# Kernel tuning notes

Hardware: AMD Instinct MI355X
Metric: run time of the kernel (lower is better)

Reference implementation:

```python
import jax, jax.numpy as jnp
import numpy as np

HIDDEN = 2048
N_HEADS = 16
N_KV_HEADS = 8
HEAD_DIM = 128  # == head_dim_original, no padding needed
ROPE_THETA = 1000000.0
EPS = 1e-6
T_NOISE = 512
T_CTX = 1536
MAX_KV = 8192


def rms_norm(x, scale, eps=EPS):
    # normalize over last axis (head_dim), per-head like nnx.RMSNorm(head_dim)
    var = jnp.mean(x * x, axis=-1, keepdims=True)
    return x * jax.lax.rsqrt(var + eps) * scale


def apply_rope(x, positions, head_dim=HEAD_DIM, theta=ROPE_THETA):
    # x: (T, N, H), positions: (T,) int
    inv_freq = 1.0 / (theta ** (jnp.arange(0, head_dim, 2, dtype=jnp.float32) / head_dim))
    ang = positions.astype(jnp.float32)[:, None] * inv_freq  # (T, H/2)
    cos = jnp.cos(ang)[:, None, :]  # (T, 1, H/2)
    sin = jnp.sin(ang)[:, None, :]
    x1, x2 = jnp.split(x, 2, axis=-1)
    return jnp.concatenate([x1 * cos - x2 * sin, x2 * cos + x1 * sin], axis=-1).astype(x.dtype)


def setup_inputs() -> dict:
    key = jax.random.key(0)
    ks = jax.random.split(key, 10)
    s = 0.02
    return {
        "x_noise": jax.random.normal(ks[0], (T_NOISE, HIDDEN), jnp.float32),
        "target_hidden": jax.random.normal(ks[1], (T_CTX, HIDDEN), jnp.float32),
        "noise_positions": jnp.arange(T_NOISE, dtype=jnp.int32) + T_CTX,
        "ctx_positions": jnp.arange(T_CTX, dtype=jnp.int32),
        "kv_cache_k": jax.random.normal(ks[2], (1, N_HEADS, MAX_KV, HEAD_DIM), jnp.float32),
        "kv_cache_v": jax.random.normal(ks[3], (1, N_HEADS, MAX_KV, HEAD_DIM), jnp.float32),
        "cache_len": 2048,
        "wq": jax.random.normal(ks[4], (HIDDEN, N_HEADS, HEAD_DIM), jnp.float32) * s,
        "wk": jax.random.normal(ks[5], (HIDDEN, N_KV_HEADS, HEAD_DIM), jnp.float32) * s,
        "wv": jax.random.normal(ks[6], (HIDDEN, N_KV_HEADS, HEAD_DIM), jnp.float32) * s,
        "wo": jax.random.normal(ks[7], (N_HEADS, HEAD_DIM, HIDDEN), jnp.float32) * s,
        "q_scale": jnp.ones((HEAD_DIM,), jnp.float32) + jax.random.uniform(ks[8], (HEAD_DIM,), jnp.float32, -0.05, 0.05),
        "k_scale": jnp.ones((HEAD_DIM,), jnp.float32) + jax.random.uniform(ks[9], (HEAD_DIM,), jnp.float32, -0.05, 0.05),
    }


def reference(x_noise, target_hidden, noise_positions, ctx_positions, kv_cache_k,
              kv_cache_v, cache_len, wq, wk, wv, wo, q_scale, k_scale):
    num_kv_groups = N_HEADS // N_KV_HEADS
    t_noise = x_noise.shape[0]

    # 1. Q projection + RMSNorm + RoPE
    q = jnp.einsum('td,dnh->tnh', x_noise, wq)
    q = rms_norm(q, q_scale)
    q = apply_rope(q, noise_positions)

    # 2. K/V over [context, noise]
    x_new = jnp.concatenate([target_hidden, x_noise], axis=0)  # (T_new, D)
    k_new = jnp.einsum('td,dkh->tkh', x_new, wk)
    v_new = jnp.einsum('td,dkh->tkh', x_new, wv)
    k_new = rms_norm(k_new, k_scale)
    new_positions = jnp.concatenate([ctx_positions, noise_positions], axis=0)
    k_new = apply_rope(k_new, new_positions)

    # 3. GQA head repeat
    if num_kv_groups > 1:
        k_new = jnp.repeat(k_new, num_kv_groups, axis=1)
        v_new = jnp.repeat(v_new, num_kv_groups, axis=1)

    # 4. Scatter new K/V into cache at dynamic offset cache_len
    t_new = x_new.shape[0]
    k_new_4d = k_new.transpose(1, 0, 2)[None]  # (1, N, T_new, H)
    v_new_4d = v_new.transpose(1, 0, 2)[None]
    kv_cache_k = jax.lax.dynamic_update_slice(kv_cache_k, k_new_4d, (0, 0, cache_len, 0))
    kv_cache_v = jax.lax.dynamic_update_slice(kv_cache_v, v_new_4d, (0, 0, cache_len, 0))
    new_cache_len = cache_len + t_new
    max_kv = kv_cache_k.shape[2]

    # 5. Non-causal attention over valid cache (segment-id mask = valid length)
    q_4d = q.transpose(1, 0, 2)[None]  # (1, N, T_noise, H)
    sm_scale = HEAD_DIM ** -0.5
    scores = jnp.einsum('bnth,bnsh->bnts', q_4d, kv_cache_k) * sm_scale  # (1,N,Tq,S)
    valid = jnp.arange(max_kv) < new_cache_len  # (S,)
    scores = jnp.where(valid[None, None, None, :], scores, jnp.float32(-1e30))
    probs = jax.nn.softmax(scores, axis=-1)
    attn = jnp.einsum('bnts,bnsh->bnth', probs, kv_cache_v)
    attn = attn[0].transpose(1, 0, 2)  # (T_noise, N, H)

    output = jnp.einsum('tnh,nhd->td', attn, wo)
    return output, kv_cache_k, kv_cache_v
```

## Files before the change

kernel.cpp:

```cpp
#include <hip/hip_runtime.h>
#include <hip/hip_bf16.h>

#define HIDDEN 2048
#define NH 16
#define NKV 8
#define HD 128
#define TN 512
#define TC 1536
#define TNEW 2048
#define MAXKV 8192

using u16 = unsigned short;
using u32 = unsigned int;

typedef short short8 __attribute__((ext_vector_type(8)));
typedef float floatx4 __attribute__((ext_vector_type(4)));

__device__ __forceinline__ u16 f2bf(float f) {
  u32 u = __float_as_uint(f);
  u += 0x7FFFu + ((u >> 16) & 1u);
  return (u16)(u >> 16);
}

__device__ __forceinline__ uint4 pack8(const float* f) {
  uint4 r;
  r.x = (u32)f2bf(f[0]) | ((u32)f2bf(f[1]) << 16);
  r.y = (u32)f2bf(f[2]) | ((u32)f2bf(f[3]) << 16);
  r.z = (u32)f2bf(f[4]) | ((u32)f2bf(f[5]) << 16);
  r.w = (u32)f2bf(f[6]) | ((u32)f2bf(f[7]) << 16);
  return r;
}

__device__ __forceinline__ short8 ldfrag(const u16* p) {
  uint4 v = *(const uint4*)p;
  return __builtin_bit_cast(short8, v);
}

__global__ __launch_bounds__(256) void cache_copy(
    const float4* __restrict__ inK, const float4* __restrict__ inV,
    float4* __restrict__ outK, float4* __restrict__ outV,
    const int* __restrict__ clp)
{
  const int cl = *clp;
  long long idx = (long long)blockIdx.x * 256 + threadIdx.x;
  const long long per = (long long)NH * MAXKV * (HD / 4);
  const float4* src = inK;
  float4* dst = outK;
  long long r = idx;
  if (r >= per) { r -= per; src = inV; dst = outV; }
  int row = (int)((r >> 5) & (MAXKV - 1));
  if (row >= cl && row < cl + TNEW) return;
  dst[r] = src[r];
}

__global__ __launch_bounds__(256) void gemm_bf16(
    const float* __restrict__ A0, int rows0, const float* __restrict__ A1,
    const float* __restrict__ B0, const float* __restrict__ B1, int Nhalf,
    float* __restrict__ C0, float* __restrict__ C1,
    int M, int N, int K, int ksteps)
{
  __shared__ u16 As[64 * 40];
  __shared__ u16 Bs[64 * 40];
  const int tid = threadIdx.x;
  const int lane = tid & 63;
  const int wave = tid >> 6;
  const int quad = lane >> 4;
  const int m16 = lane & 15;
  const int bm = blockIdx.y * 64;
  const int bn = blockIdx.x * 64;
  const int wm = (wave >> 1) * 32;
  const int wn = (wave & 1) * 32;
  const int z = blockIdx.z;
  const int kbase = z * ksteps * 32;

  const float* B = (bn < Nhalf) ? B0 : B1;
  float*       C = (bn < Nhalf) ? C0 : C1;
  const int n0 = (bn < Nhalf) ? bn : bn - Nhalf;
  const int strideN = (bn < Nhalf) ? Nhalf : (N - Nhalf);

  floatx4 acc[2][2];
#pragma unroll
  for (int i = 0; i < 2; i++)
#pragma unroll
    for (int j = 0; j < 2; j++)
#pragma unroll
      for (int r = 0; r < 4; r++) acc[i][j][r] = 0.0f;

  const int arow = tid >> 2, akg = (tid & 3) * 8;
  const int brow = tid >> 3, bng = (tid & 7) * 8;
  const int garow = bm + arow;
  const float* Ap = (garow < rows0) ? (A0 + (size_t)garow * K)
                                    : (A1 + (size_t)(garow - rows0) * K);

  for (int ks = 0; ks < ksteps; ks++) {
    const int k0 = kbase + ks * 32;
    if (k0 >= K) break;
    float av[8];
    *(float4*)(av)     = *(const float4*)(Ap + k0 + akg);
    *(float4*)(av + 4) = *(const float4*)(Ap + k0 + akg + 4);
    *(uint4*)&As[arow * 40 + akg] = pack8(av);

    float bv[8];
    const float* Bp = B + (size_t)(k0 + brow) * strideN + n0 + bng;
    *(float4*)(bv)     = *(const float4*)(Bp);
    *(float4*)(bv + 4) = *(const float4*)(Bp + 4);
#pragma unroll
    for (int j = 0; j < 8; j++) Bs[(bng + j) * 40 + brow] = f2bf(bv[j]);

    __syncthreads();

    short8 a0 = ldfrag(&As[(wm + m16) * 40 + quad * 8]);
    short8 a1 = ldfrag(&As[(wm + 16 + m16) * 40 + quad * 8]);
    short8 b0 = ldfrag(&Bs[(wn + m16) * 40 + quad * 8]);
    short8 b1 = ldfrag(&Bs[(wn + 16 + m16) * 40 + quad * 8]);
    acc[0][0] = __builtin_amdgcn_mfma_f32_16x16x32_bf16(a0, b0, acc[0][0], 0, 0, 0);
    acc[0][1] = __builtin_amdgcn_mfma_f32_16x16x32_bf16(a0, b1, acc[0][1], 0, 0, 0);
    acc[1][0] = __builtin_amdgcn_mfma_f32_16x16x32_bf16(a1, b0, acc[1][0], 0, 0, 0);
    acc[1][1] = __builtin_amdgcn_mfma_f32_16x16x32_bf16(a1, b1, acc[1][1], 0, 0, 0);

    __syncthreads();
  }

  const size_t zoff = (size_t)z * M * Nhalf;
#pragma unroll
  for (int mt = 0; mt < 2; mt++)
#pragma unroll
    for (int nt = 0; nt < 2; nt++)
#pragma unroll
      for (int r = 0; r < 4; r++) {
        int row = bm + wm + mt * 16 + quad * 4 + r;
        int col = wn + nt * 16 + m16;
        C[zoff + (size_t)row * strideN + n0 + col] = acc[mt][nt][r];
      }
}

__global__ __launch_bounds__(256) void reduce4(
    const float4* __restrict__ P, float4* __restrict__ C, int n4)
{
  int idx = blockIdx.x * 256 + threadIdx.x;
  if (idx >= n4) return;
  float4 a = P[idx], b = P[idx + n4], c = P[idx + 2 * n4], d = P[idx + 3 * n4];
  float4 r;
  r.x = (a.x + b.x) + (c.x + d.x);
  r.y = (a.y + b.y) + (c.y + d.y);
  r.z = (a.z + b.z) + (c.z + d.z);
  r.w = (a.w + b.w) + (c.w + d.w);
  C[idx] = r;
}

__global__ __launch_bounds__(64) void q_post_k(
    const float* __restrict__ qproj, const int* __restrict__ npos,
    const float* __restrict__ qscale, u16* __restrict__ qbf)
{
  const int t = blockIdx.x, n = blockIdx.y, i = threadIdx.x;
  const size_t base = (size_t)t * HIDDEN + n * HD;
  const float x1 = qproj[base + i];
  const float x2 = qproj[base + i + 64];
  float ss = x1 * x1 + x2 * x2;
#pragma unroll
  for (int m = 1; m < 64; m <<= 1) ss += __shfl_xor(ss, m, 64);
  const float rstd = rsqrtf(ss * (1.0f / HD) + 1e-6f);
  float y1 = x1 * rstd * qscale[i];
  float y2 = x2 * rstd * qscale[i + 64];
  const float pos = (float)npos[t];
  const float ang = pos * exp2f(-(float)i * (19.931568569324174f / 64.0f));
  const float c = cosf(ang), s = sinf(ang);
  const float sc = 0.08838834764831845f * 1.4426950408889634f;
  qbf[base + i]      = f2bf((y1 * c - y2 * s) * sc);
  qbf[base + i + 64] = f2bf((y2 * c + y1 * s) * sc);
}

__global__ __launch_bounds__(64) void k_post_k(
    const float* __restrict__ kproj, const int* __restrict__ ctxpos,
    const int* __restrict__ npos, const float* __restrict__ kscale,
    const int* __restrict__ clp, float* __restrict__ outK)
{
  const int t = blockIdx.x, kh = blockIdx.y, i = threadIdx.x;
  const int cl = *clp;
  const size_t base = (size_t)t * (NKV * HD) + kh * HD;
  const float x1 = kproj[base + i];
  const float x2 = kproj[base + i + 64];
  float ss = x1 * x1 + x2 * x2;
#pragma unroll
  for (int m = 1; m < 64; m <<= 1) ss += __shfl_xor(ss, m, 64);
  const float rstd = rsqrtf(ss * (1.0f / HD) + 1e-6f);
  float y1 = x1 * rstd * kscale[i];
  float y2 = x2 * rstd * kscale[i + 64];
  const int posi = (t < TC) ? ctxpos[t] : npos[t - TC];
  const float ang = (float)posi * exp2f(-(float)i * (19.931568569324174f / 64.0f));
  const float c = cosf(ang), s = sinf(ang);
  const float o1 = y1 * c - y2 * s;
  const float o2 = y2 * c + y1 * s;
  const size_t row = (size_t)cl + t;
  const size_t b0 = ((size_t)(2 * kh) * MAXKV + row) * HD;
  const size_t b1 = ((size_t)(2 * kh + 1) * MAXKV + row) * HD;
  outK[b0 + i] = o1; outK[b0 + i + 64] = o2;
  outK[b1 + i] = o1; outK[b1 + i + 64] = o2;
}

__global__ __launch_bounds__(128) void v_post_k(
    const float* __restrict__ vproj, const int* __restrict__ clp,
    float* __restrict__ outV)
{
  const int t = blockIdx.x, kh = blockIdx.y, h = threadIdx.x;
  const int cl = *clp;
  const float v = vproj[(size_t)t * (NKV * HD) + kh * HD + h];
  const size_t row = (size_t)cl + t;
  outV[((size_t)(2 * kh) * MAXKV + row) * HD + h] = v;
  outV[((size_t)(2 * kh + 1) * MAXKV + row) * HD + h] = v;
}

__global__ __launch_bounds__(256) void attn_k(
    const u16* __restrict__ qbf, const float* __restrict__ outK,
    const float* __restrict__ outV, const int* __restrict__ clp,
    float* __restrict__ Opart, float* __restrict__ Oml)
{
  __shared__ u16 Ks[32 * 136];
  __shared__ u16 Vt[128 * 40];
  __shared__ u16 Ps[4 * 16 * 40];
  const int tid = threadIdx.x;
  const int lane = tid & 63, wave = tid >> 6;
  const int quad = lane >> 4, m16 = lane & 15;
  const int head = blockIdx.y;
  const int qbase = blockIdx.x * 64 + wave * 16;
  const int z = blockIdx.z, splits = gridDim.z;
  const int Svalid = *clp + TNEW;
  const int ntiles = (Svalid + 31) >> 5;
  const int per = (ntiles + splits - 1) / splits;
  const int it0 = z * per;
  const int it1 = min(ntiles, it0 + per);

  short8 qf[4];
#pragma unroll
  for (int kb = 0; kb < 4; kb++)
    qf[kb] = ldfrag(&qbf[((size_t)(qbase + m16) * NH + head) * HD + kb * 32 + quad * 8]);

  floatx4 O[8];
#pragma unroll
  for (int i = 0; i < 8; i++)
#pragma unroll
    for (int r = 0; r < 4; r++) O[i][r] = 0.0f;
  float mrow[4], lrow[4];
#pragma unroll
  for (int r = 0; r < 4; r++) { mrow[r] = -1e30f; lrow[r] = 0.0f; }

  const int sstage = tid >> 3;
  const int hg = (tid & 7) * 16;

  for (int it = it0; it < it1; it++) {
    const int s0 = it * 32;
    {
      int srow = s0 + sstage; if (srow > MAXKV - 1) srow = MAXKV - 1;
      const float* kp = outK + ((size_t)head * MAXKV + srow) * HD + hg;
      float tv[16];
      *(float4*)(tv)      = *(const float4*)(kp);
      *(float4*)(tv + 4)  = *(const float4*)(kp + 4);
      *(float4*)(tv + 8)  = *(const float4*)(kp + 8);
      *(float4*)(tv + 12) = *(const float4*)(kp + 12);
      *(uint4*)&Ks[sstage * 136 + hg]     = pack8(tv);
      *(uint4*)&Ks[sstage * 136 + hg + 8] = pack8(tv + 8);
      const float* vp = outV + ((size_t)head * MAXKV + srow) * HD + hg;
      float vv[16];
      *(float4*)(vv)      = *(const float4*)(vp);
      *(float4*)(vv + 4)  = *(const float4*)(vp + 4);
      *(float4*)(vv + 8)  = *(const float4*)(vp + 8);
      *(float4*)(vv + 12) = *(const float4*)(vp + 12);
#pragma unroll
      for (int j = 0; j < 16; j++) Vt[(hg + j) * 40 + sstage] = f2bf(vv[j]);
    }
    __syncthreads();

    floatx4 sc[2];
#pragma unroll
    for (int st = 0; st < 2; st++) {
      floatx4 a;
#pragma unroll
      for (int r = 0; r < 4; r++) a[r] = 0.0f;
#pragma unroll
      for (int kb = 0; kb < 4; kb++) {
        short8 kf = ldfrag(&Ks[(st * 16 + m16) * 136 + kb * 32 + quad * 8]);
        a = __builtin_amdgcn_mfma_f32_16x16x32_bf16(qf[kb], kf, a, 0, 0, 0);
      }
      const int scol = s0 + st * 16 + m16;
      if (scol >= Svalid) {
#pragma unroll
        for (int r = 0; r < 4; r++) a[r] = -1e30f;
      }
      sc[st] = a;
    }

    float alpha[4];
#pragma unroll
    for (int r = 0; r < 4; r++) {
      float mx = fmaxf(sc[0][r], sc[1][r]);
      mx = fmaxf(mx, __shfl_xor(mx, 1, 64));
      mx = fmaxf(mx, __shfl_xor(mx, 2, 64));
      mx = fmaxf(mx, __shfl_xor(mx, 4, 64));
      mx = fmaxf(mx, __shfl_xor(mx, 8, 64));
      const float mn = fmaxf(mrow[r], mx);
      alpha[r] = exp2f(mrow[r] - mn);
      const float p0 = exp2f(sc[0][r] - mn);
      const float p1 = exp2f(sc[1][r] - mn);
      sc[0][r] = p0; sc[1][r] = p1;
      float rs = p0 + p1;
      rs += __shfl_xor(rs, 1, 64);
      rs += __shfl_xor(rs, 2, 64);
      rs += __shfl_xor(rs, 4, 64);
      rs += __shfl_xor(rs, 8, 64);
      lrow[r] = lrow[r] * alpha[r] + rs;
      mrow[r] = mn;
    }
#pragma unroll
    for (int hb = 0; hb < 8; hb++)
#pragma unroll
      for (int r = 0; r < 4; r++) O[hb][r] *= alpha[r];

    u16* myPs = &Ps[wave * 640];
#pragma unroll
    for (int st = 0; st < 2; st++)
#pragma unroll
      for (int r = 0; r < 4; r++)
        myPs[(quad * 4 + r) * 40 + st * 16 + m16] = f2bf(sc[st][r]);
    short8 pf = ldfrag(&myPs[m16 * 40 + quad * 8]);
#pragma unroll
    for (int hb = 0; hb < 8; hb++) {
      short8 vf = ldfrag(&Vt[(hb * 16 + m16) * 40 + quad * 8]);
      O[hb] = __builtin_amdgcn_mfma_f32_16x16x32_bf16(pf, vf, O[hb], 0, 0, 0);
    }
    __syncthreads();
  }

  const size_t zbase = (size_t)z * TN * NH;
  const int trow = qbase + quad * 4;
#pragma unroll
  for (int hb = 0; hb < 8; hb++)
#pragma unroll
    for (int r = 0; r < 4; r++)
      Opart[(zbase + (size_t)(trow + r) * NH + head) * HD + hb * 16 + m16] = O[hb][r];
  if (m16 == 0) {
#pragma unroll
    for (int r = 0; r < 4; r++) {
      Oml[(zbase + (size_t)(trow + r) * NH + head) * 2 + 0] = mrow[r];
      Oml[(zbase + (size_t)(trow + r) * NH + head) * 2 + 1] = lrow[r];
    }
  }
}

__global__ __launch_bounds__(128) void attn_combine(
    const float* __restrict__ Opart, const float* __restrict__ Oml,
    float* __restrict__ attnb, int splits)
{
  const int pair = blockIdx.x;
  const int h = threadIdx.x;
  float M = -1e30f;
  for (int zz = 0; zz < splits; zz++)
    M = fmaxf(M, Oml[((size_t)zz * TN * NH + pair) * 2]);
  float l = 0.0f, o = 0.0f;
  for (int zz = 0; zz < splits; zz++) {
    const float mi = Oml[((size_t)zz * TN * NH + pair) * 2];
    const float li = Oml[((size_t)zz * TN * NH + pair) * 2 + 1];
    const float w = exp2f(mi - M);
    l += li * w;
    o += Opart[((size_t)zz * TN * NH + pair) * HD + h] * w;
  }
  attnb[(size_t)pair * HD + h] = o / l;
}

extern "C" void kernel_launch(void* const* d_in, const int* in_sizes, int n_in,
                              void* d_out, int out_size, void* d_ws, size_t ws_size,
                              hipStream_t stream) {
  const float* x_noise       = (const float*)d_in[0];
  const float* target_hidden = (const float*)d_in[1];
  const int*   noise_pos     = (const int*)d_in[2];
  const int*   ctx_pos       = (const int*)d_in[3];
  const float* inK           = (const float*)d_in[4];
  const float* inV           = (const float*)d_in[5];
  const int*   cache_len     = (const int*)d_in[6];
  const float* wq            = (const float*)d_in[7];
  const float* wk            = (const float*)d_in[8];
  const float* wv            = (const float*)d_in[9];
  const float* wo            = (const float*)d_in[10];
  const float* q_scale       = (const float*)d_in[11];
  const float* k_scale       = (const float*)d_in[12];

  float* out0 = (float*)d_out;
  float* outK = out0 + (size_t)TN * HIDDEN;
  float* outV = outK + (size_t)NH * MAXKV * HD;

  size_t off = 0;
  auto walloc = [&](size_t bytes) -> void* {
    void* p = (char*)d_ws + off;
    off += (bytes + 255) & ~(size_t)255;
    return p;
  };
  u16*   qbf   = (u16*)walloc((size_t)TN * HIDDEN * 2);
  float* attnb = (float*)walloc((size_t)TN * HIDDEN * 4);
  float* qproj = (float*)walloc((size_t)TN * HIDDEN * 4);
  float* kproj = (float*)walloc((size_t)TNEW * NKV * HD * 4);
  float* vproj = (float*)walloc((size_t)TNEW * NKV * HD * 4);
  float* scratch = (float*)((char*)d_ws + off);
  const size_t avail = (ws_size > off) ? (ws_size - off) : 0;

  const size_t per_split = (size_t)TN * NH * HD * 4 + (size_t)TN * NH * 8;
  int asplits = 2;
  if (avail >= 8 * per_split) asplits = 8;
  else if (avail >= 4 * per_split) asplits = 4;
  float* Opart = scratch;
  float* Oml   = Opart + (size_t)asplits * TN * NH * HD;

  const bool ksplit = (avail >= (size_t)4 * TN * HIDDEN * 4);
  float* gpart = scratch;

  cache_copy<<<dim3(32768), dim3(256), 0, stream>>>(
      (const float4*)inK, (const float4*)inV, (float4*)outK, (float4*)outV, cache_len);

  if (ksplit) {
    gemm_bf16<<<dim3(HIDDEN / 64, TN / 64, 4), dim3(256), 0, stream>>>(
        x_noise, TN, x_noise, wq, wq, HIDDEN, gpart, gpart, TN, HIDDEN, HIDDEN, 16);
    reduce4<<<dim3((TN * HIDDEN / 4 + 255) / 256), dim3(256), 0, stream>>>(
        (const float4*)gpart, (float4*)qproj, TN * HIDDEN / 4);
  } else {
    gemm_bf16<<<dim3(HIDDEN / 64, TN / 64, 1), dim3(256), 0, stream>>>(
        x_noise, TN, x_noise, wq, wq, HIDDEN, qproj, qproj, TN, HIDDEN, HIDDEN, 64);
  }

  gemm_bf16<<<dim3(2 * NKV * HD / 64, TNEW / 64, 1), dim3(256), 0, stream>>>(
      target_hidden, TC, x_noise, wk, wv, NKV * HD, kproj, vproj,
      TNEW, 2 * NKV * HD, HIDDEN, 64);

  q_post_k<<<dim3(TN, NH), dim3(64), 0, stream>>>(qproj, noise_pos, q_scale, qbf);
  k_post_k<<<dim3(TNEW, NKV), dim3(64), 0, stream>>>(
      kproj, ctx_pos, noise_pos, k_scale, cache_len, outK);
  v_post_k<<<dim3(TNEW, NKV), dim3(128), 0, stream>>>(vproj, cache_len, outV);

  attn_k<<<dim3(TN / 64, NH, asplits), dim3(256), 0, stream>>>(
      qbf, outK, outV, cache_len, Opart, Oml);
  attn_combine<<<dim3(TN * NH), dim3(128), 0, stream>>>(Opart, Oml, attnb, asplits);

  if (ksplit) {
    gemm_bf16<<<dim3(HIDDEN / 64, TN / 64, 4), dim3(256), 0, stream>>>(
        attnb, TN, attnb, wo, wo, HIDDEN, gpart, gpart, TN, HIDDEN, HIDDEN, 16);
    reduce4<<<dim3((TN * HIDDEN / 4 + 255) / 256), dim3(256), 0, stream>>>(
        (const float4*)gpart, (float4*)out0, TN * HIDDEN / 4);
  } else {
    gemm_bf16<<<dim3(HIDDEN / 64, TN / 64, 1), dim3(256), 0, stream>>>(
        attnb, TN, attnb, wo, wo, HIDDEN, out0, out0, TN, HIDDEN, HIDDEN, 64);
  }
}
```

Baseline: 556.4 us.

## Build bf16 K and transposed-V shadow caches and use double-buffered async attention

The cache copy and the K/V post-processing kernels now also write bf16 shadow copies of the cache: K stays row-major and V is transposed. A new attention kernel streams these shadows straight into LDS with global_load_lds, double-buffered with manual waitcnt and barriers, an XOR-swizzled K layout and a remapped block order for locality. This halves attention read traffic and removes the per-tile fp32-to-bf16 conversion and transpose. The cost is extra shadow writes, scattered 2-byte transposed V stores in the copy kernel, and a workspace requirement large enough for two shadow buffers, with a fallback to the old path when it is not available.

```diff
diff --git a/kernel.cpp b/kernel.cpp
--- a/kernel.cpp
+++ b/kernel.cpp
@@ -36,21 +36,46 @@
   return __builtin_bit_cast(short8, v);
 }
 
+__device__ __forceinline__ void gload16(const void* g, void* l) {
+  __builtin_amdgcn_global_load_lds(
+      (const __attribute__((address_space(1))) u32*)g,
+      (__attribute__((address_space(3))) u32*)l, 16, 0, 0);
+}
+
 __global__ __launch_bounds__(256) void cache_copy(
     const float4* __restrict__ inK, const float4* __restrict__ inV,
     float4* __restrict__ outK, float4* __restrict__ outV,
-    const int* __restrict__ clp)
+    const int* __restrict__ clp, u16* __restrict__ Kb, u16* __restrict__ VbT)
 {
   const int cl = *clp;
   long long idx = (long long)blockIdx.x * 256 + threadIdx.x;
   const long long per = (long long)NH * MAXKV * (HD / 4);
-  const float4* src = inK;
-  float4* dst = outK;
+  const float4* src; float4* dst; bool isv;
   long long r = idx;
-  if (r >= per) { r -= per; src = inV; dst = outV; }
+  if (r < per) { src = inK; dst = outK; isv = false; }
+  else { r -= per; src = inV; dst = outV; isv = true; }
   int row = (int)((r >> 5) & (MAXKV - 1));
   if (row >= cl && row < cl + TNEW) return;
-  dst[r] = src[r];
+  float4 v = src[r];
+  dst[r] = v;
+  if (row < cl) {
+    if (!isv) {
+      if (Kb) {
+        uint2 p;
+        p.x = (u32)f2bf(v.x) | ((u32)f2bf(v.y) << 16);
+        p.y = (u32)f2bf(v.z) | ((u32)f2bf(v.w) << 16);
+        *(uint2*)(Kb + (size_t)r * 4) = p;
+      }
+    } else if (VbT) {
+      int head = (int)(r >> 18);
+      int h0 = ((int)r & 31) * 4;
+      size_t basev = ((size_t)head * HD + h0) * MAXKV + row;
+      VbT[basev]             = f2bf(v.x);
+      VbT[basev + MAXKV]     = f2bf(v.y);
+      VbT[basev + 2 * MAXKV] = f2bf(v.z);
+      VbT[basev + 3 * MAXKV] = f2bf(v.w);
+    }
+  }
 }
 
 __global__ __launch_bounds__(256) void gemm_bf16(
@@ -173,7 +198,7 @@
 __global__ __launch_bounds__(64) void k_post_k(
     const float* __restrict__ kproj, const int* __restrict__ ctxpos,
     const int* __restrict__ npos, const float* __restrict__ kscale,
-    const int* __restrict__ clp, float* __restrict__ outK)
+    const int* __restrict__ clp, float* __restrict__ outK, u16* __restrict__ Kb)
 {
   const int t = blockIdx.x, kh = blockIdx.y, i = threadIdx.x;
   const int cl = *clp;
@@ -196,11 +221,16 @@
   const size_t b1 = ((size_t)(2 * kh + 1) * MAXKV + row) * HD;
   outK[b0 + i] = o1; outK[b0 + i + 64] = o2;
   outK[b1 + i] = o1; outK[b1 + i + 64] = o2;
+  if (Kb) {
+    const u16 s1 = f2bf(o1), s2 = f2bf(o2);
+    Kb[b0 + i] = s1; Kb[b0 + i + 64] = s2;
+    Kb[b1 + i] = s1; Kb[b1 + i + 64] = s2;
+  }
 }
 
 __global__ __launch_bounds__(128) void v_post_k(
     const float* __restrict__ vproj, const int* __restrict__ clp,
-    float* __restrict__ outV)
+    float* __restrict__ outV, u16* __restrict__ VbT)
 {
   const int t = blockIdx.x, kh = blockIdx.y, h = threadIdx.x;
   const int cl = *clp;
@@ -208,6 +238,174 @@
   const size_t row = (size_t)cl + t;
   outV[((size_t)(2 * kh) * MAXKV + row) * HD + h] = v;
   outV[((size_t)(2 * kh + 1) * MAXKV + row) * HD + h] = v;
+  if (VbT) {
+    const u16 vb = f2bf(v);
+    VbT[((size_t)(2 * kh) * HD + h) * MAXKV + row] = vb;
+    VbT[((size_t)(2 * kh + 1) * HD + h) * MAXKV + row] = vb;
+  }
+}
+
+__global__ __launch_bounds__(256) void attn_sh(
+    const u16* __restrict__ qbf, const u16* __restrict__ Kb,
+    const u16* __restrict__ VbT, const int* __restrict__ clp,
+    float* __restrict__ Opart, float* __restrict__ Oml, int splits)
+{
+  __shared__ u16 Ks[2][32 * 128];
+  __shared__ u16 Vt[2][128 * 32];
+  __shared__ u16 Ps[4][16 * 40];
+
+  const int tid = threadIdx.x;
+  const int lane = tid & 63, wave = tid >> 6;
+  const int quad = lane >> 4, m16 = lane & 15;
+
+  const int lin = blockIdx.x;
+  const int ppx = (NH * splits) >> 3;
+  const int c = lin & 7;
+  const int jj = lin >> 3;
+  const int pair = c * ppx + (jj % ppx);
+  const int x = jj / ppx;
+  const int head = pair & (NH - 1);
+  const int z = pair >> 4;
+
+  const int qbase = x * 64 + wave * 16;
+  const int Svalid = *clp + TNEW;
+  const int ntiles = (Svalid + 31) >> 5;
+  const int per = (ntiles + splits - 1) / splits;
+  const int it0 = z * per;
+  const int it1 = (ntiles < it0 + per) ? ntiles : (it0 + per);
+
+  short8 qf[4];
+#pragma unroll
+  for (int kb = 0; kb < 4; kb++)
+    qf[kb] = ldfrag(&qbf[((size_t)(qbase + m16) * NH + head) * HD + kb * 32 + quad * 8]);
+
+  floatx4 O[8];
+#pragma unroll
+  for (int i = 0; i < 8; i++)
+#pragma unroll
+    for (int r = 0; r < 4; r++) O[i][r] = 0.0f;
+  float mrow[4], lrow[4];
+#pragma unroll
+  for (int r = 0; r < 4; r++) { mrow[r] = -1e30f; lrow[r] = 0.0f; }
+
+  const int krow = tid >> 4;
+  const int ksrccol = ((tid & 15) * 16) ^ ((krow & 7) << 4);
+  const char* Kbase = (const char*)(Kb + (size_t)head * MAXKV * HD);
+  const int vh = tid >> 2;
+  const int vs8 = (tid & 3) * 8;
+  const char* Vbase = (const char*)(VbT + (size_t)head * HD * MAXKV);
+  u16* myPs = &Ps[wave][0];
+  const int kxor = (m16 & 7) << 4;
+  const int wb = wave * 512;
+
+  int b = 0;
+  if (it0 < it1) {
+    {
+      const int s0 = it0 * 32;
+      gload16(Kbase + ((size_t)(s0 + krow) << 8) + ksrccol,          &Ks[0][wb]);
+      gload16(Kbase + ((size_t)(s0 + krow + 16) << 8) + ksrccol,     &Ks[0][2048 + wb]);
+      gload16(Vbase + (((size_t)vh * MAXKV + s0 + vs8) << 1),        &Vt[0][wb]);
+      gload16(Vbase + (((size_t)(vh + 64) * MAXKV + s0 + vs8) << 1), &Vt[0][2048 + wb]);
+    }
+    for (int it = it0; it < it1; ++it) {
+      if (it + 1 < it1) {
+        const int s1 = (it + 1) * 32;
+        u16* KsN = &Ks[b ^ 1][0];
+        u16* VtN = &Vt[b ^ 1][0];
+        gload16(Kbase + ((size_t)(s1 + krow) << 8) + ksrccol,          KsN + wb);
+        gload16(Kbase + ((size_t)(s1 + krow + 16) << 8) + ksrccol,     KsN + 2048 + wb);
+        gload16(Vbase + (((size_t)vh * MAXKV + s1 + vs8) << 1),        VtN + wb);
+        gload16(Vbase + (((size_t)(vh + 64) * MAXKV + s1 + vs8) << 1), VtN + 2048 + wb);
+        asm volatile("s_waitcnt vmcnt(4) lgkmcnt(0)" ::: "memory");
+      } else {
+        asm volatile("s_waitcnt vmcnt(0) lgkmcnt(0)" ::: "memory");
+      }
+      __builtin_amdgcn_s_barrier();
+      __builtin_amdgcn_sched_barrier(0);
+
+      const u16* KsB = &Ks[b][0];
+      const u16* VtB = &Vt[b][0];
+      const int s0 = it * 32;
+
+      floatx4 sc[2];
+#pragma unroll
+      for (int st = 0; st < 2; st++) {
+        floatx4 a;
+#pragma unroll
+        for (int r = 0; r < 4; r++) a[r] = 0.0f;
+        const int rofs = (st * 16 + m16) * 128;
+#pragma unroll
+        for (int kb = 0; kb < 4; kb++) {
+          short8 kf = ldfrag(&KsB[rofs + (((kb * 64 + quad * 16) ^ kxor) >> 1)]);
+          a = __builtin_amdgcn_mfma_f32_16x16x32_bf16(qf[kb], kf, a, 0, 0, 0);
+        }
+        const int scol = s0 + st * 16 + m16;
+        if (scol >= Svalid) {
+#pragma unroll
+          for (int r = 0; r < 4; r++) a[r] = -1e30f;
+        }
+        sc[st] = a;
+      }
+
+      float alpha[4];
+#pragma unroll
+      for (int r = 0; r < 4; r++) {
+        float mx = fmaxf(sc[0][r], sc[1][r]);
+        mx = fmaxf(mx, __shfl_xor(mx, 1, 64));
+        mx = fmaxf(mx, __shfl_xor(mx, 2, 64));
+        mx = fmaxf(mx, __shfl_xor(mx, 4, 64));
+        mx = fmaxf(mx, __shfl_xor(mx, 8, 64));
+        const float mn = fmaxf(mrow[r], mx);
+        alpha[r] = exp2f(mrow[r] - mn);
+        const float p0 = exp2f(sc[0][r] - mn);
+        const float p1 = exp2f(sc[1][r] - mn);
+        sc[0][r] = p0; sc[1][r] = p1;
+        float rs = p0 + p1;
+        rs += __shfl_xor(rs, 1, 64);
+        rs += __shfl_xor(rs, 2, 64);
+        rs += __shfl_xor(rs, 4, 64);
+        rs += __shfl_xor(rs, 8, 64);
+        lrow[r] = lrow[r] * alpha[r] + rs;
+        mrow[r] = mn;
+      }
+#pragma unroll
+      for (int hb = 0; hb < 8; hb++)
+#pragma unroll
+        for (int r = 0; r < 4; r++) O[hb][r] *= alpha[r];
+
+#pragma unroll
+      for (int st = 0; st < 2; st++)
+#pragma unroll
+        for (int r = 0; r < 4; r++)
+          myPs[(quad * 4 + r) * 40 + st * 16 + m16] = f2bf(sc[st][r]);
+      short8 pfr = ldfrag(&myPs[m16 * 40 + quad * 8]);
+#pragma unroll
+      for (int hb = 0; hb < 8; hb++) {
+        short8 vf = ldfrag(&VtB[(hb * 16 + m16) * 32 + quad * 8]);
+        O[hb] = __builtin_amdgcn_mfma_f32_16x16x32_bf16(pfr, vf, O[hb], 0, 0, 0);
+      }
+
+      asm volatile("s_waitcnt lgkmcnt(0)" ::: "memory");
+      __builtin_amdgcn_s_barrier();
+      __builtin_amdgcn_sched_barrier(0);
+      b ^= 1;
+    }
+  }
+
+  const size_t zbase = (size_t)z * TN * NH;
+  const int trow = qbase + quad * 4;
+#pragma unroll
+  for (int hb = 0; hb < 8; hb++)
+#pragma unroll
+    for (int r = 0; r < 4; r++)
+      Opart[(zbase + (size_t)(trow + r) * NH + head) * HD + hb * 16 + m16] = O[hb][r];
+  if (m16 == 0) {
+#pragma unroll
+    for (int r = 0; r < 4; r++) {
+      Oml[(zbase + (size_t)(trow + r) * NH + head) * 2 + 0] = mrow[r];
+      Oml[(zbase + (size_t)(trow + r) * NH + head) * 2 + 1] = lrow[r];
+    }
+  }
 }
 
 __global__ __launch_bounds__(256) void attn_k(
@@ -215,9 +413,9 @@
     const float* __restrict__ outV, const int* __restrict__ clp,
     float* __restrict__ Opart, float* __restrict__ Oml)
 {
-  __shared__ u16 Ks[32 * 136];
-  __shared__ u16 Vt[128 * 40];
-  __shared__ u16 Ps[4 * 16 * 40];
+  __shared__ u16 Ksl[32 * 136];
+  __shared__ u16 Vtl[128 * 40];
+  __shared__ u16 Psl[4 * 16 * 40];
   const int tid = threadIdx.x;
   const int lane = tid & 63, wave = tid >> 6;
   const int quad = lane >> 4, m16 = lane & 15;
@@ -257,8 +455,8 @@
       *(float4*)(tv + 4)  = *(const float4*)(kp + 4);
       *(float4*)(tv + 8)  = *(const float4*)(kp + 8);
       *(float4*)(tv + 12) = *(const float4*)(kp + 12);
-      *(uint4*)&Ks[sstage * 136 + hg]     = pack8(tv);
-      *(uint4*)&Ks[sstage * 136 + hg + 8] = pack8(tv + 8);
+      *(uint4*)&Ksl[sstage * 136 + hg]     = pack8(tv);
+      *(uint4*)&Ksl[sstage * 136 + hg + 8] = pack8(tv + 8);
       const float* vp = outV + ((size_t)head * MAXKV + srow) * HD + hg;
       float vv[16];
       *(float4*)(vv)      = *(const float4*)(vp);
@@ -266,7 +464,7 @@
       *(float4*)(vv + 8)  = *(const float4*)(vp + 8);
       *(float4*)(vv + 12) = *(const float4*)(vp + 12);
 #pragma unroll
-      for (int j = 0; j < 16; j++) Vt[(hg + j) * 40 + sstage] = f2bf(vv[j]);
+      for (int j = 0; j < 16; j++) Vtl[(hg + j) * 40 + sstage] = f2bf(vv[j]);
     }
     __syncthreads();
 
@@ -278,7 +476,7 @@
       for (int r = 0; r < 4; r++) a[r] = 0.0f;
 #pragma unroll
       for (int kb = 0; kb < 4; kb++) {
-        short8 kf = ldfrag(&Ks[(st * 16 + m16) * 136 + kb * 32 + quad * 8]);
+        short8 kf = ldfrag(&Ksl[(st * 16 + m16) * 136 + kb * 32 + quad * 8]);
         a = __builtin_amdgcn_mfma_f32_16x16x32_bf16(qf[kb], kf, a, 0, 0, 0);
       }
       const int scol = s0 + st * 16 + m16;
@@ -315,7 +513,7 @@
 #pragma unroll
       for (int r = 0; r < 4; r++) O[hb][r] *= alpha[r];
 
-    u16* myPs = &Ps[wave * 640];
+    u16* myPs = &Psl[wave * 640];
 #pragma unroll
     for (int st = 0; st < 2; st++)
 #pragma unroll
@@ -324,7 +522,7 @@
     short8 pf = ldfrag(&myPs[m16 * 40 + quad * 8]);
 #pragma unroll
     for (int hb = 0; hb < 8; hb++) {
-      short8 vf = ldfrag(&Vt[(hb * 16 + m16) * 40 + quad * 8]);
+      short8 vf = ldfrag(&Vtl[(hb * 16 + m16) * 40 + quad * 8]);
       O[hb] = __builtin_amdgcn_mfma_f32_16x16x32_bf16(pf, vf, O[hb], 0, 0, 0);
     }
     __syncthreads();
@@ -398,21 +596,38 @@
   float* qproj = (float*)walloc((size_t)TN * HIDDEN * 4);
   float* kproj = (float*)walloc((size_t)TNEW * NKV * HD * 4);
   float* vproj = (float*)walloc((size_t)TNEW * NKV * HD * 4);
+
+  const size_t PER_SPLIT = (size_t)TN * NH * HD * 4 + (size_t)TN * NH * 8;
+  const size_t SHB = (size_t)NH * MAXKV * HD * sizeof(u16);
+  const size_t GPART = (size_t)4 * TN * HIDDEN * 4;
+  auto maxsz = [](size_t a, size_t b) { return a > b ? a : b; };
+
+  size_t avail = (ws_size > off) ? ws_size - off : 0;
+  u16 *Kb = nullptr, *VbT = nullptr;
+  int asplits = 0;
+  if (avail >= 2 * SHB + maxsz(8 * PER_SPLIT, GPART))       asplits = 8;
+  else if (avail >= 2 * SHB + maxsz(4 * PER_SPLIT, GPART))  asplits = 4;
+  const bool shadow = (asplits > 0);
+  if (shadow) {
+    Kb  = (u16*)walloc(SHB);
+    VbT = (u16*)walloc(SHB);
+  }
+
   float* scratch = (float*)((char*)d_ws + off);
-  const size_t avail = (ws_size > off) ? (ws_size - off) : 0;
-
-  const size_t per_split = (size_t)TN * NH * HD * 4 + (size_t)TN * NH * 8;
-  int asplits = 2;
-  if (avail >= 8 * per_split) asplits = 8;
-  else if (avail >= 4 * per_split) asplits = 4;
+  const size_t avail2 = (ws_size > off) ? ws_size - off : 0;
+  if (!shadow) {
+    asplits = 2;
+    if (avail2 >= 8 * PER_SPLIT) asplits = 8;
+    else if (avail2 >= 4 * PER_SPLIT) asplits = 4;
+  }
   float* Opart = scratch;
   float* Oml   = Opart + (size_t)asplits * TN * NH * HD;
-
-  const bool ksplit = (avail >= (size_t)4 * TN * HIDDEN * 4);
+  const bool ksplit = (avail2 >= GPART);
   float* gpart = scratch;
 
   cache_copy<<<dim3(32768), dim3(256), 0, stream>>>(
-      (const float4*)inK, (const float4*)inV, (float4*)outK, (float4*)outV, cache_len);
+      (const float4*)inK, (const float4*)inV, (float4*)outK, (float4*)outV,
+      cache_len, Kb, VbT);
 
   if (ksplit) {
     gemm_bf16<<<dim3(HIDDEN / 64, TN / 64, 4), dim3(256), 0, stream>>>(
@@ -430,11 +645,16 @@
 
   q_post_k<<<dim3(TN, NH), dim3(64), 0, stream>>>(qproj, noise_pos, q_scale, qbf);
   k_post_k<<<dim3(TNEW, NKV), dim3(64), 0, stream>>>(
-      kproj, ctx_pos, noise_pos, k_scale, cache_len, outK);
-  v_post_k<<<dim3(TNEW, NKV), dim3(128), 0, stream>>>(vproj, cache_len, outV);
-
-  attn_k<<<dim3(TN / 64, NH, asplits), dim3(256), 0, stream>>>(
-      qbf, outK, outV, cache_len, Opart, Oml);
+      kproj, ctx_pos, noise_pos, k_scale, cache_len, outK, Kb);
+  v_post_k<<<dim3(TNEW, NKV), dim3(128), 0, stream>>>(vproj, cache_len, outV, VbT);
+
+  if (shadow) {
+    attn_sh<<<dim3((TN / 64) * NH * asplits), dim3(256), 0, stream>>>(
+        qbf, Kb, VbT, cache_len, Opart, Oml, asplits);
+  } else {
+    attn_k<<<dim3(TN / 64, NH, asplits), dim3(256), 0, stream>>>(
+        qbf, outK, outV, cache_len, Opart, Oml);
+  }
   attn_combine<<<dim3(TN * NH), dim3(128), 0, stream>>>(Opart, Oml, attnb, asplits);
 
   if (ksplit) {
```

After: 565.6 us. About the same (+1.6%).
